# Kernel optimization log

Measured on AMD Instinct MI355X. Metric: run time of the kernel, lower is better.

The kernel has to match this reference:

```python
import jax, jax.numpy as jnp
import numpy as np

B, S, D, F, T, NS, L, H = 8, 1024, 1024, 4096, 64, 512, 32, 16
TAG_RATE = 0.5      # config.tagging_rate
GSR = 0.5           # config.gate_scaling_rate
ATT_EPS = 1e-12     # config.layer_norm_eps (att_norm)
ENC_EPS = 1e-5      # torch TransformerEncoderLayer default


def _ln(x, g, b, eps):
    m = x.mean(-1, keepdims=True)
    v = x.var(-1, keepdims=True)
    return (x - m) * jax.lax.rsqrt(v + eps) * g + b


def _rope(x):
    # standard rotary embedding over the full hidden dim
    d = x.shape[-1]
    s = x.shape[1]
    inv = 1.0 / (10000.0 ** (jnp.arange(0, d, 2, dtype=jnp.float32) / d))
    ang = jnp.arange(s, dtype=jnp.float32)[:, None] * inv[None, :]  # [S, D/2]
    sin, cos = jnp.sin(ang), jnp.cos(ang)
    x1, x2 = x[..., 0::2], x[..., 1::2]
    return jnp.stack([x1 * cos - x2 * sin, x1 * sin + x2 * cos], axis=-1).reshape(x.shape)


def setup_inputs() -> dict:
    key = jax.random.key(0)
    ks = jax.random.split(key, 24)
    p = lambda k, shp: (0.02 * jax.random.normal(k, shp, dtype=jnp.float32))
    inp = {
        'word_embedding': jax.random.normal(ks[0], (B, S, D), dtype=jnp.float32),
        'attention_mask': jnp.ones((B, S), dtype=jnp.int32),
        'span_batch': jax.random.randint(ks[1], (NS,), 0, B, dtype=jnp.int32),
        'span_start': jax.random.randint(ks[2], (NS,), 0, S - L, dtype=jnp.int32),
        'span_tag': jax.random.randint(ks[3], (NS,), 0, T, dtype=jnp.int32),
        'tag_emb': p(ks[4], (T, D)),
        'gate_w': p(ks[5], (D, 1)),
        'gate_b': jnp.zeros((1,), jnp.float32),
        'attn_ln_g': jnp.ones((D,), jnp.float32),
        'attn_ln_b': jnp.zeros((D,), jnp.float32),
        'in_proj_w': p(ks[6], (3 * D, D)),
        'in_proj_b': jnp.zeros((3 * D,), jnp.float32),
        'out_proj_w': p(ks[7], (D, D)),
        'out_proj_b': jnp.zeros((D,), jnp.float32),
        'enc_ln1_g': jnp.ones((D,), jnp.float32),
        'enc_ln1_b': jnp.zeros((D,), jnp.float32),
        'lin1_w': p(ks[8], (F, D)),
        'lin1_b': jnp.zeros((F,), jnp.float32),
        'lin2_w': p(ks[9], (D, F)),
        'lin2_b': jnp.zeros((D,), jnp.float32),
        'enc_ln2_g': jnp.ones((D,), jnp.float32),
        'enc_ln2_b': jnp.zeros((D,), jnp.float32),
    }
    return inp


def _mha(x, pad, in_proj_w, in_proj_b, out_proj_w, out_proj_b):
    b, s, d = x.shape
    hd = d // H
    qkv = x @ in_proj_w.T + in_proj_b                       # [B,S,3D]
    q, k, v = jnp.split(qkv, 3, axis=-1)
    rs = lambda t: t.reshape(b, s, H, hd).transpose(0, 2, 1, 3)  # [B,H,S,hd]
    q, k, v = rs(q), rs(k), rs(v)
    scores = jnp.einsum('bhqd,bhkd->bhqk', q, k) / jnp.sqrt(jnp.float32(hd))
    scores = jnp.where(pad[:, None, None, :], jnp.float32(-1e30), scores)
    attn = jax.nn.softmax(scores, axis=-1)
    o = jnp.einsum('bhqk,bhkd->bhqd', attn, v).transpose(0, 2, 1, 3).reshape(b, s, d)
    return o @ out_proj_w.T + out_proj_b


def reference(word_embedding, attention_mask, span_batch, span_start, span_tag,
              tag_emb, gate_w, gate_b, attn_ln_g, attn_ln_b,
              in_proj_w, in_proj_b, out_proj_w, out_proj_b,
              enc_ln1_g, enc_ln1_b, lin1_w, lin1_b, lin2_w, lin2_b,
              enc_ln2_g, enc_ln2_b):
    raw = word_embedding                        # dropout off (eval)
    we = _rope(word_embedding)
    # ragged gather -> gate -> scatter-add over fixed-length spans
    tok = span_start[:, None] + jnp.arange(L, dtype=jnp.int32)[None, :]  # [NS,L]
    X = we[span_batch[:, None], tok]            # [NS,L,D]
    gate = GSR * jax.nn.sigmoid(X @ gate_w + gate_b) + (1.0 - GSR) / 2.0  # [NS,L,1]
    res = gate * tag_emb[span_tag][:, None, :] * jnp.float32(L)          # [NS,L,D]
    taged = jnp.zeros_like(word_embedding).at[span_batch[:, None], tok].add(res)
    out_emb = raw + taged * TAG_RATE            # if_merge_by_add
    out_emb = _ln(out_emb, attn_ln_g, attn_ln_b, ATT_EPS)
    pad = attention_mask == 0
    # torch TransformerEncoderLayer (post-norm, relu)
    a = _mha(out_emb, pad, in_proj_w, in_proj_b, out_proj_w, out_proj_b)
    x = _ln(out_emb + a, enc_ln1_g, enc_ln1_b, ENC_EPS)
    ff = jax.nn.relu(x @ lin1_w.T + lin1_b) @ lin2_w.T + lin2_b
    enc = _ln(x + ff, enc_ln2_g, enc_ln2_b, ENC_EPS)
    return enc + out_emb
```

## Files before the change

### kernel.cpp

```cpp
#include <hip/hip_runtime.h>

#define DEV __device__ __forceinline__

typedef short bf16x8 __attribute__((ext_vector_type(8)));
typedef float f32x4 __attribute__((ext_vector_type(4)));
typedef unsigned short u16;
typedef unsigned int u32;

typedef __attribute__((address_space(3))) void lds_void;
typedef __attribute__((address_space(1))) void gbl_void;

DEV void async_copy16(void* lds_dst, const void* g_src) {
    __builtin_amdgcn_global_load_lds((gbl_void*)g_src, (lds_void*)lds_dst, 16, 0, 0);
}

DEV u16 f2bf(float x) {
    u32 u = __float_as_uint(x);
    return (u16)((u + 0x7fffu + ((u >> 16) & 1u)) >> 16);
}
DEV u16 f2bf_fast(float x) {
    return (u16)((__float_as_uint(x) + 0x8000u) >> 16);
}
DEV float bf2f(u16 v) { return __uint_as_float(((u32)v) << 16); }

__global__ __launch_bounds__(256) void f2bf_kernel(const float* __restrict__ src,
                                                   u16* __restrict__ dst, int n4) {
    const int i = blockIdx.x * 256 + threadIdx.x;
    if (i < n4) {
        const float4 v = ((const float4*)src)[i];
        ushort4 o;
        o.x = f2bf(v.x); o.y = f2bf(v.y); o.z = f2bf(v.z); o.w = f2bf(v.w);
        ((ushort4*)dst)[i] = o;
    }
}

__global__ __launch_bounds__(256) void span_kernel(
    const float* __restrict__ we, const int* __restrict__ sb,
    const int* __restrict__ ss, const int* __restrict__ stg,
    const float* __restrict__ tag_emb, const float* __restrict__ gate_w,
    const float* __restrict__ gate_b, float* __restrict__ out_pre) {
    __shared__ float red[4];
    const int n = blockIdx.x >> 5;
    const int l = blockIdx.x & 31;
    const int t = threadIdx.x;
    const int b = sb[n];
    const int s = ss[n] + l;
    const int tag = stg[n];
    const long base = ((long)b * 1024 + s) * 1024;
    float dot = 0.f;
#pragma unroll
    for (int pp = 0; pp < 2; ++pp) {
        const int p = t + pp * 256;
        const float e1 = we[base + 2 * p];
        const float e2 = we[base + 2 * p + 1];
        const float inv = exp2f((float)p * (-13.287712379549449f / 512.0f));
        const float ang = (float)s * inv;
        const float sa = sinf(ang), ca = cosf(ang);
        const float r1 = e1 * ca - e2 * sa;
        const float r2 = e1 * sa + e2 * ca;
        dot += r1 * gate_w[2 * p] + r2 * gate_w[2 * p + 1];
    }
#pragma unroll
    for (int off = 32; off > 0; off >>= 1) dot += __shfl_xor(dot, off, 64);
    if ((t & 63) == 0) red[t >> 6] = dot;
    __syncthreads();
    const float z = red[0] + red[1] + red[2] + red[3] + gate_b[0];
    const float gate = 0.25f + 0.5f / (1.f + __expf(-z));
    const float coef = gate * 16.f;
    const float* te = tag_emb + (long)tag * 1024;
#pragma unroll
    for (int c = 0; c < 4; ++c) {
        const int d = t + c * 256;
        atomicAdd(&out_pre[base + d], coef * te[d]);
    }
}

template <bool WRITE_F32, bool WRITE_BF, bool FINAL>
__global__ __launch_bounds__(256) void ln_kernel(
    const float* __restrict__ X, const float* __restrict__ g,
    const float* __restrict__ bta, float eps, float* __restrict__ Yf,
    u16* __restrict__ Ybf, const u16* __restrict__ addend) {
    __shared__ float red[8];
    const long row = blockIdx.x;
    const int t = threadIdx.x;
    const float4 x = ((const float4*)(X + row * 1024))[t];
    float s = x.x + x.y + x.z + x.w;
#pragma unroll
    for (int off = 32; off > 0; off >>= 1) s += __shfl_xor(s, off, 64);
    if ((t & 63) == 0) red[t >> 6] = s;
    __syncthreads();
    const float mean = (red[0] + red[1] + red[2] + red[3]) * (1.f / 1024.f);
    float4 dx;
    dx.x = x.x - mean; dx.y = x.y - mean; dx.z = x.z - mean; dx.w = x.w - mean;
    float ss = dx.x * dx.x + dx.y * dx.y + dx.z * dx.z + dx.w * dx.w;
#pragma unroll
    for (int off = 32; off > 0; off >>= 1) ss += __shfl_xor(ss, off, 64);
    if ((t & 63) == 0) red[4 + (t >> 6)] = ss;
    __syncthreads();
    const float var = (red[4] + red[5] + red[6] + red[7]) * (1.f / 1024.f);
    const float rstd = rsqrtf(var + eps);
    const float4 gv = ((const float4*)g)[t];
    const float4 bv = ((const float4*)bta)[t];
    float4 y;
    y.x = dx.x * rstd * gv.x + bv.x;
    y.y = dx.y * rstd * gv.y + bv.y;
    y.z = dx.z * rstd * gv.z + bv.z;
    y.w = dx.w * rstd * gv.w + bv.w;
    if (FINAL) {
        const ushort4 a = ((const ushort4*)(addend + row * 1024))[t];
        y.x += bf2f(a.x); y.y += bf2f(a.y); y.z += bf2f(a.z); y.w += bf2f(a.w);
    }
    if (WRITE_F32) ((float4*)(Yf + row * 1024))[t] = y;
    if (WRITE_BF) {
        ushort4 o;
        o.x = f2bf(y.x); o.y = f2bf(y.y); o.z = f2bf(y.z); o.w = f2bf(y.w);
        ((ushort4*)(Ybf + row * 1024))[t] = o;
    }
}

template <bool OUT_BF16, bool RELU, bool HAS_RES>
__global__ __launch_bounds__(256, 2) void gemm_nt(
    const u16* __restrict__ A, const u16* __restrict__ B,
    const float* __restrict__ bias, const u16* __restrict__ res,
    void* __restrict__ Cout, int N, int K) {
    __shared__ u16 Al[8192];
    __shared__ u16 Bl[8192];
    const int tid = threadIdx.x;
    const int wave = tid >> 6;
    const int lane = tid & 63;
    const int quad = lane >> 4;
    const int lq = lane & 15;
    const int wm = wave >> 1;
    const int wn = wave & 1;
    const long rowBase = (long)blockIdx.x * 128;
    const long colBase = (long)blockIdx.y * 128;

    f32x4 acc[4][4];
    const f32x4 fzero = {0.f, 0.f, 0.f, 0.f};
#pragma unroll
    for (int i = 0; i < 4; ++i)
#pragma unroll
        for (int j = 0; j < 4; ++j) acc[i][j] = fzero;

    const int rX = tid >> 3;
    const int pX = (tid & 7) ^ (rX & 7);
    const u16* gA = A + (rowBase + rX) * (long)K + pX * 8;
    const u16* gB = B + (colBase + rX) * (long)K + pX * 8;
    u16* ldsA = Al + wave * 512;
    u16* ldsB = Bl + wave * 512;

    for (int kt = 0; kt < K; kt += 64) {
        __syncthreads();
#pragma unroll
        for (int c = 0; c < 4; ++c) {
            async_copy16(ldsA + c * 2048, gA + (long)c * 32 * K + kt);
            async_copy16(ldsB + c * 2048, gB + (long)c * 32 * K + kt);
        }
        __syncthreads();
#pragma unroll
        for (int ks = 0; ks < 2; ++ks) {
            bf16x8 af[4], bfr[4];
#pragma unroll
            for (int i = 0; i < 4; ++i) {
                const int r = wm * 64 + i * 16 + lq;
                af[i] = *(const bf16x8*)&Al[r * 64 + (((ks * 4 + quad) ^ (lq & 7)) * 8)];
            }
#pragma unroll
            for (int j = 0; j < 4; ++j) {
                const int r = wn * 64 + j * 16 + lq;
                bfr[j] = *(const bf16x8*)&Bl[r * 64 + (((ks * 4 + quad) ^ (lq & 7)) * 8)];
            }
#pragma unroll
            for (int i = 0; i < 4; ++i)
#pragma unroll
                for (int j = 0; j < 4; ++j)
                    acc[i][j] = __builtin_amdgcn_mfma_f32_16x16x32_bf16(
                        af[i], bfr[j], acc[i][j], 0, 0, 0);
        }
    }

    float biasv[4];
#pragma unroll
    for (int j = 0; j < 4; ++j) biasv[j] = bias[colBase + wn * 64 + j * 16 + lq];
#pragma unroll
    for (int i = 0; i < 4; ++i) {
        const long grow = rowBase + wm * 64 + i * 16 + quad * 4;
#pragma unroll
        for (int j = 0; j < 4; ++j) {
            const long gcol = colBase + wn * 64 + j * 16 + lq;
#pragma unroll
            for (int r = 0; r < 4; ++r) {
                float v = acc[i][j][r] + biasv[j];
                if (RELU) v = fmaxf(v, 0.f);
                if (HAS_RES) v += bf2f(res[(grow + r) * N + gcol]);
                if (OUT_BF16)
                    ((u16*)Cout)[(grow + r) * N + gcol] = f2bf(v);
                else
                    ((float*)Cout)[(grow + r) * N + gcol] = v;
            }
        }
    }
}

#define PH_SYNC()                                          \
    do {                                                   \
        __builtin_amdgcn_s_barrier();                      \
        asm volatile("s_waitcnt lgkmcnt(0)" ::: "memory"); \
        __builtin_amdgcn_sched_barrier(0);                 \
    } while (0)

template <bool RELU>
__global__ __launch_bounds__(512, 2) void gemm_nt8(
    const u16* __restrict__ A, const u16* __restrict__ B,
    const float* __restrict__ bias, u16* __restrict__ Cout, int N, int K) {
    __shared__ u16 Al[2][16384];
    __shared__ u16 Bl[2][16384];
    const int tid = threadIdx.x;
    const int wave = tid >> 6;
    const int lane = tid & 63;
    const int quad = lane >> 4;
    const int lq = lane & 15;
    const int lq7 = lq & 7;
    const int wm = wave >> 2;
    const int wn = wave & 3;
    const long rowBase = (long)blockIdx.x * 256;
    const long colBase = (long)blockIdx.y * 256;
    const int NT = K >> 6;

    const int rs = tid >> 3;
    const int js = (tid & 7) ^ (rs & 7);
    const u16* gA = A + (rowBase + rs) * (long)K + js * 8;
    const u16* gB = B + (colBase + rs) * (long)K + js * 8;

    f32x4 acc[8][4];
    const f32x4 fz = {0.f, 0.f, 0.f, 0.f};
#pragma unroll
    for (int i = 0; i < 8; ++i)
#pragma unroll
        for (int j = 0; j < 4; ++j) acc[i][j] = fz;

    auto stA = [&](int buf, int h, int t) {
        u16* d = &Al[buf][h * 8192 + wave * 512];
        const u16* s = gA + (long)h * 128 * K + t * 64;
        async_copy16(d, s);
        async_copy16(d + 4096, s + (long)64 * K);
    };
    auto stB = [&](int buf, int h, int t) {
        u16* d = &Bl[buf][h * 8192 + wave * 512];
        const u16* s = gB + (long)h * 128 * K + t * 64;
        async_copy16(d, s);
        async_copy16(d + 4096, s + (long)64 * K);
    };
    auto ldA = [&](int buf, int i, int kh) {
        const int r = wm * 128 + i * 16 + lq;
        return *(const bf16x8*)&Al[buf][r * 64 + ((((kh << 2) | quad) ^ lq7) << 3)];
    };
    auto ldB = [&](int buf, int j, int kh) {
        const int r = wn * 64 + j * 16 + lq;
        return *(const bf16x8*)&Bl[buf][r * 64 + ((((kh << 2) | quad) ^ lq7) << 3)];
    };

    stA(0, 0, 0); stA(0, 1, 0); stB(0, 0, 0); stB(0, 1, 0);
    stA(1, 0, 1);
    asm volatile("s_waitcnt vmcnt(2)" ::: "memory");
    __builtin_amdgcn_s_barrier();

    bf16x8 at[8], ab[8], bl[4], br[4];
    for (int it = 0; it < (NT >> 1); ++it) {
        const int t1 = 2 * it + 1;
        int t2 = 2 * it + 2; if (t2 >= NT) t2 -= NT;
        int t3 = 2 * it + 3; if (t3 >= NT) t3 -= NT;

#pragma unroll
        for (int i = 0; i < 4; ++i) { at[2 * i] = ldA(0, i, 0); at[2 * i + 1] = ldA(0, i, 1); }
#pragma unroll
        for (int j = 0; j < 2; ++j) { bl[2 * j] = ldB(0, j, 0); bl[2 * j + 1] = ldB(0, j, 1); }
        stA(1, 1, t1);
        PH_SYNC();
        __builtin_amdgcn_s_setprio(1);
#pragma unroll
        for (int i = 0; i < 4; ++i)
#pragma unroll
            for (int j = 0; j < 2; ++j)
#pragma unroll
                for (int kh = 0; kh < 2; ++kh)
                    acc[i][j] = __builtin_amdgcn_mfma_f32_16x16x32_bf16(
                        at[2 * i + kh], bl[2 * j + kh], acc[i][j], 0, 0, 0);
        __builtin_amdgcn_s_setprio(0);
        __builtin_amdgcn_s_barrier();
#pragma unroll
        for (int j = 0; j < 2; ++j) { br[2 * j] = ldB(0, j + 2, 0); br[2 * j + 1] = ldB(0, j + 2, 1); }
        stB(1, 0, t1);
        PH_SYNC();
        __builtin_amdgcn_s_setprio(1);
#pragma unroll
        for (int i = 0; i < 4; ++i)
#pragma unroll
            for (int j = 0; j < 2; ++j)
#pragma unroll
                for (int kh = 0; kh < 2; ++kh)
                    acc[i][j + 2] = __builtin_amdgcn_mfma_f32_16x16x32_bf16(
                        at[2 * i + kh], br[2 * j + kh], acc[i][j + 2], 0, 0, 0);
        __builtin_amdgcn_s_setprio(0);
        __builtin_amdgcn_s_barrier();
#pragma unroll
        for (int i = 0; i < 4; ++i) { ab[2 * i] = ldA(0, i + 4, 0); ab[2 * i + 1] = ldA(0, i + 4, 1); }
        stB(1, 1, t1);
        PH_SYNC();
        __builtin_amdgcn_s_setprio(1);
#pragma unroll
        for (int i = 0; i < 4; ++i)
#pragma unroll
            for (int j = 0; j < 2; ++j)
#pragma unroll
                for (int kh = 0; kh < 2; ++kh)
                    acc[i + 4][j] = __builtin_amdgcn_mfma_f32_16x16x32_bf16(
                        ab[2 * i + kh], bl[2 * j + kh], acc[i + 4][j], 0, 0, 0);
        __builtin_amdgcn_s_setprio(0);
        __builtin_amdgcn_s_barrier();
        stA(0, 0, t2);
        PH_SYNC();
        __builtin_amdgcn_s_setprio(1);
#pragma unroll
        for (int i = 0; i < 4; ++i)
#pragma unroll
            for (int j = 0; j < 2; ++j)
#pragma unroll
                for (int kh = 0; kh < 2; ++kh)
                    acc[i + 4][j + 2] = __builtin_amdgcn_mfma_f32_16x16x32_bf16(
                        ab[2 * i + kh], br[2 * j + kh], acc[i + 4][j + 2], 0, 0, 0);
        __builtin_amdgcn_s_setprio(0);
        asm volatile("s_waitcnt vmcnt(2)" ::: "memory");
        __builtin_amdgcn_s_barrier();

#pragma unroll
        for (int i = 0; i < 4; ++i) { at[2 * i] = ldA(1, i, 0); at[2 * i + 1] = ldA(1, i, 1); }
#pragma unroll
        for (int j = 0; j < 2; ++j) { bl[2 * j] = ldB(1, j, 0); bl[2 * j + 1] = ldB(1, j, 1); }
        stA(0, 1, t2);
        PH_SYNC();
        __builtin_amdgcn_s_setprio(1);
#pragma unroll
        for (int i = 0; i < 4; ++i)
#pragma unroll
            for (int j = 0; j < 2; ++j)
#pragma unroll
                for (int kh = 0; kh < 2; ++kh)
                    acc[i][j] = __builtin_amdgcn_mfma_f32_16x16x32_bf16(
                        at[2 * i + kh], bl[2 * j + kh], acc[i][j], 0, 0, 0);
        __builtin_amdgcn_s_setprio(0);
        __builtin_amdgcn_s_barrier();
#pragma unroll
        for (int j = 0; j < 2; ++j) { br[2 * j] = ldB(1, j + 2, 0); br[2 * j + 1] = ldB(1, j + 2, 1); }
        stB(0, 0, t2);
        PH_SYNC();
        __builtin_amdgcn_s_setprio(1);
#pragma unroll
        for (int i = 0; i < 4; ++i)
#pragma unroll
            for (int j = 0; j < 2; ++j)
#pragma unroll
                for (int kh = 0; kh < 2; ++kh)
                    acc[i][j + 2] = __builtin_amdgcn_mfma_f32_16x16x32_bf16(
                        at[2 * i + kh], br[2 * j + kh], acc[i][j + 2], 0, 0, 0);
        __builtin_amdgcn_s_setprio(0);
        __builtin_amdgcn_s_barrier();
#pragma unroll
        for (int i = 0; i < 4; ++i) { ab[2 * i] = ldA(1, i + 4, 0); ab[2 * i + 1] = ldA(1, i + 4, 1); }
        stB(0, 1, t2);
        PH_SYNC();
        __builtin_amdgcn_s_setprio(1);
#pragma unroll
        for (int i = 0; i < 4; ++i)
#pragma unroll
            for (int j = 0; j < 2; ++j)
#pragma unroll
                for (int kh = 0; kh < 2; ++kh)
                    acc[i + 4][j] = __builtin_amdgcn_mfma_f32_16x16x32_bf16(
                        ab[2 * i + kh], bl[2 * j + kh], acc[i + 4][j], 0, 0, 0);
        __builtin_amdgcn_s_setprio(0);
        __builtin_amdgcn_s_barrier();
        stA(1, 0, t3);
        PH_SYNC();
        __builtin_amdgcn_s_setprio(1);
#pragma unroll
        for (int i = 0; i < 4; ++i)
#pragma unroll
            for (int j = 0; j < 2; ++j)
#pragma unroll
                for (int kh = 0; kh < 2; ++kh)
                    acc[i + 4][j + 2] = __builtin_amdgcn_mfma_f32_16x16x32_bf16(
                        ab[2 * i + kh], br[2 * j + kh], acc[i + 4][j + 2], 0, 0, 0);
        __builtin_amdgcn_s_setprio(0);
        asm volatile("s_waitcnt vmcnt(2)" ::: "memory");
        __builtin_amdgcn_s_barrier();
    }

    asm volatile("s_waitcnt vmcnt(0)" ::: "memory");
    float bv[4];
#pragma unroll
    for (int j = 0; j < 4; ++j) bv[j] = bias[colBase + wn * 64 + j * 16 + lq];
#pragma unroll
    for (int i = 0; i < 8; ++i) {
        const long grow = rowBase + wm * 128 + i * 16 + quad * 4;
#pragma unroll
        for (int j = 0; j < 4; ++j) {
            const long gcol = colBase + wn * 64 + j * 16 + lq;
#pragma unroll
            for (int r = 0; r < 4; ++r) {
                float v = acc[i][j][r] + bv[j];
                if (RELU) v = fmaxf(v, 0.f);
                Cout[(grow + r) * N + gcol] = f2bf(v);
            }
        }
    }
}

__global__ __launch_bounds__(256) void vtrans_kernel(const u16* __restrict__ QKV,
                                                     u16* __restrict__ Vt) {
    __shared__ u16 tile[64][72];
    const int bid = blockIdx.x;
    const int st = bid & 15;
    const int h = (bid >> 4) & 15;
    const int b = bid >> 8;
    const int t = threadIdx.x;
    const int sl = t >> 2;
    const int dc = (t & 3) * 16;
    const u16* src = QKV + ((long)(b * 1024 + st * 64 + sl)) * 3072 + 2048 + h * 64 + dc;
    *(uint4*)&tile[sl][dc] = *(const uint4*)src;
    *(uint4*)&tile[sl][dc + 8] = *(const uint4*)(src + 8);
    __syncthreads();
    const int dl = t >> 2;
    const int sc = (t & 3) * 16;
    union { u16 u[16]; uint4 q[2]; } tmp;
#pragma unroll
    for (int i = 0; i < 16; ++i) tmp.u[i] = tile[sc + i][dl];
    u16* dst = Vt + ((long)(b * 16 + h) * 64 + dl) * 1024 + st * 64 + sc;
    *(uint4*)dst = tmp.q[0];
    *(uint4*)(dst + 8) = tmp.q[1];
}

__global__ __launch_bounds__(256, 4) void attn_kernel(
    const u16* __restrict__ QKV, const u16* __restrict__ Vt,
    const int* __restrict__ mask, u16* __restrict__ Out) {
    __shared__ u16 KL[4096];
    __shared__ u16 VL[4096];
    __shared__ u16 PL[4][16 * 72];
    const int tid = threadIdx.x;
    const int wid = tid >> 6;
    const int lane = tid & 63;
    const int quad = lane >> 4;
    const int lq = lane & 15;
    const int slot0 = quad ^ (lq & 7);
    const int slot1 = slot0 ^ 4;

    const int bid = blockIdx.x;
    const int qb = bid & 7;
    const int h = (bid >> 3) & 15;
    const int b = bid >> 7;
    const int qbase = qb * 128 + wid * 32;

    bf16x8 aq[2][2];
#pragma unroll
    for (int t = 0; t < 2; ++t) {
        const u16* qp = QKV + ((long)(b * 1024 + qbase + t * 16 + lq)) * 3072 +
                        h * 64 + quad * 8;
        aq[t][0] = *(const bf16x8*)qp;
        aq[t][1] = *(const bf16x8*)(qp + 32);
    }

    const int c0 = tid, c1 = 256 + tid;
    const int r0 = c0 >> 3, j0 = (c0 & 7) ^ (r0 & 7);
    const int r1 = c1 >> 3, j1 = (c1 & 7) ^ (r1 & 7);
    const u16* srcK0 = QKV + ((long)(b * 1024 + r0)) * 3072 + 1024 + h * 64 + j0 * 8;
    const u16* srcK1 = QKV + ((long)(b * 1024 + r1)) * 3072 + 1024 + h * 64 + j1 * 8;
    const u16* srcV0 = Vt + ((long)(b * 16 + h) * 64 + r0) * 1024 + j0 * 8;
    const u16* srcV1 = Vt + ((long)(b * 16 + h) * 64 + r1) * 1024 + j1 * 8;
    u16* ldsK0 = KL + wid * 512;
    u16* ldsK1 = KL + 2048 + wid * 512;
    u16* ldsV0 = VL + wid * 512;
    u16* ldsV1 = VL + 2048 + wid * 512;

    const f32x4 fzero = {0.f, 0.f, 0.f, 0.f};
    f32x4 acc[2][4];
#pragma unroll
    for (int t = 0; t < 2; ++t)
#pragma unroll
        for (int j = 0; j < 4; ++j) acc[t][j] = fzero;
    float lsum[2][4] = {{0.f, 0.f, 0.f, 0.f}, {0.f, 0.f, 0.f, 0.f}};
    u16* myP = PL[wid];
    const int* mrow = mask + b * 1024;

    for (int kt = 0; kt < 1024; kt += 64) {
        __syncthreads();
        async_copy16(ldsK0, srcK0 + (long)kt * 3072);
        async_copy16(ldsK1, srcK1 + (long)kt * 3072);
        async_copy16(ldsV0, srcV0 + kt);
        async_copy16(ldsV1, srcV1 + kt);
        __syncthreads();

        bf16x8 kf0[4], kf1[4];
#pragma unroll
        for (int ct = 0; ct < 4; ++ct) {
            const int rowb = (ct * 16 + lq) * 64;
            kf0[ct] = *(const bf16x8*)&KL[rowb + slot0 * 8];
            kf1[ct] = *(const bf16x8*)&KL[rowb + slot1 * 8];
        }
        float mw[4];
#pragma unroll
        for (int ct = 0; ct < 4; ++ct) mw[ct] = mrow[kt + ct * 16 + lq] ? 1.f : 0.f;

#pragma unroll
        for (int t = 0; t < 2; ++t) {
            f32x4 s[4];
#pragma unroll
            for (int ct = 0; ct < 4; ++ct) {
                s[ct] = __builtin_amdgcn_mfma_f32_16x16x32_bf16(aq[t][0], kf0[ct],
                                                                fzero, 0, 0, 0);
                s[ct] = __builtin_amdgcn_mfma_f32_16x16x32_bf16(aq[t][1], kf1[ct],
                                                                s[ct], 0, 0, 0);
            }
            asm volatile("s_waitcnt lgkmcnt(0)" ::: "memory");
#pragma unroll
            for (int ct = 0; ct < 4; ++ct)
#pragma unroll
                for (int r = 0; r < 4; ++r) {
                    const float p = mw[ct] * __expf(s[ct][r] * 0.125f);
                    lsum[t][r] += p;
                    myP[(quad * 4 + r) * 72 + ct * 16 + lq] = f2bf_fast(p);
                }
            asm volatile("s_waitcnt lgkmcnt(0)" ::: "memory");
            const bf16x8 pf0 = *(const bf16x8*)&myP[lq * 72 + quad * 8];
            const bf16x8 pf1 = *(const bf16x8*)&myP[lq * 72 + 32 + quad * 8];
#pragma unroll
            for (int j = 0; j < 4; ++j) {
                const int rowb = (j * 16 + lq) * 64;
                const bf16x8 vf0 = *(const bf16x8*)&VL[rowb + slot0 * 8];
                const bf16x8 vf1 = *(const bf16x8*)&VL[rowb + slot1 * 8];
                acc[t][j] = __builtin_amdgcn_mfma_f32_16x16x32_bf16(pf0, vf0,
                                                                    acc[t][j], 0, 0, 0);
                acc[t][j] = __builtin_amdgcn_mfma_f32_16x16x32_bf16(pf1, vf1,
                                                                    acc[t][j], 0, 0, 0);
            }
        }
    }

#pragma unroll
    for (int t = 0; t < 2; ++t) {
        float inv[4];
#pragma unroll
        for (int r = 0; r < 4; ++r) {
            float l = lsum[t][r];
#pragma unroll
            for (int off = 1; off < 16; off <<= 1) l += __shfl_xor(l, off, 16);
            inv[r] = 1.f / l;
        }
        const long orow = (long)b * 1024 + qbase + t * 16 + quad * 4;
#pragma unroll
        for (int j = 0; j < 4; ++j)
#pragma unroll
            for (int r = 0; r < 4; ++r)
                Out[(orow + r) * 1024 + h * 64 + j * 16 + lq] =
                    f2bf_fast(acc[t][j][r] * inv[r]);
    }
}

extern "C" void kernel_launch(void* const* d_in, const int* in_sizes, int n_in,
                              void* d_out, int out_size, void* d_ws, size_t ws_size,
                              hipStream_t stream) {
    const float* we        = (const float*)d_in[0];
    const int*   amask     = (const int*)d_in[1];
    const int*   span_b    = (const int*)d_in[2];
    const int*   span_s    = (const int*)d_in[3];
    const int*   span_t    = (const int*)d_in[4];
    const float* tag_emb   = (const float*)d_in[5];
    const float* gate_w    = (const float*)d_in[6];
    const float* gate_b    = (const float*)d_in[7];
    const float* attn_ln_g = (const float*)d_in[8];
    const float* attn_ln_b = (const float*)d_in[9];
    const float* in_proj_w = (const float*)d_in[10];
    const float* in_proj_b = (const float*)d_in[11];
    const float* out_proj_w= (const float*)d_in[12];
    const float* out_proj_b= (const float*)d_in[13];
    const float* enc1_g    = (const float*)d_in[14];
    const float* enc1_b    = (const float*)d_in[15];
    const float* lin1_w    = (const float*)d_in[16];
    const float* lin1_b    = (const float*)d_in[17];
    const float* lin2_w    = (const float*)d_in[18];
    const float* lin2_b    = (const float*)d_in[19];
    const float* enc2_g    = (const float*)d_in[20];
    const float* enc2_b    = (const float*)d_in[21];
    float* out = (float*)d_out;

    char* ws = (char*)d_ws;
    size_t off = 0;
    auto alloc = [&](size_t bytes) {
        void* p = ws + off;
        off += (bytes + 255) & ~(size_t)255;
        return p;
    };
    const size_t MT = 8192;
    u16* oe_bf   = (u16*)alloc(MT * 1024 * 2);
    u16* ax_bf   = (u16*)alloc(MT * 1024 * 2);
    char* region = (char*)alloc((size_t)67108864);
    u16* qkv_bf  = (u16*)region;
    u16* vt_bf   = (u16*)(region + (size_t)MT * 3072 * 2);
    u16* ff1_bf  = (u16*)region;
    u16* wb_inproj  = (u16*)alloc((size_t)3072 * 1024 * 2);
    u16* wb_outproj = (u16*)alloc((size_t)1024 * 1024 * 2);
    u16* wb_lin1    = (u16*)alloc((size_t)4096 * 1024 * 2);
    u16* wb_lin2    = (u16*)alloc((size_t)1024 * 4096 * 2);

    hipMemcpyAsync(out, we, MT * 1024 * 4, hipMemcpyDeviceToDevice, stream);
    f2bf_kernel<<<3072, 256, 0, stream>>>(in_proj_w, wb_inproj, 3072 * 1024 / 4);
    f2bf_kernel<<<1024, 256, 0, stream>>>(out_proj_w, wb_outproj, 1024 * 1024 / 4);
    f2bf_kernel<<<4096, 256, 0, stream>>>(lin1_w, wb_lin1, 4096 * 1024 / 4);
    f2bf_kernel<<<4096, 256, 0, stream>>>(lin2_w, wb_lin2, 1024 * 4096 / 4);
    span_kernel<<<16384, 256, 0, stream>>>(we, span_b, span_s, span_t, tag_emb,
                                           gate_w, gate_b, out);
    ln_kernel<false, true, false><<<8192, 256, 0, stream>>>(
        out, attn_ln_g, attn_ln_b, 1e-12f, nullptr, oe_bf, nullptr);
    dim3 g1(32, 12);
    gemm_nt8<false><<<g1, 512, 0, stream>>>(oe_bf, wb_inproj, in_proj_b,
                                            qkv_bf, 3072, 1024);
    vtrans_kernel<<<2048, 256, 0, stream>>>(qkv_bf, vt_bf);
    attn_kernel<<<1024, 256, 0, stream>>>(qkv_bf, vt_bf, amask, ax_bf);
    dim3 g2(64, 8);
    gemm_nt<false, false, true><<<g2, 256, 0, stream>>>(ax_bf, wb_outproj, out_proj_b,
                                                        oe_bf, out, 1024, 1024);
    ln_kernel<false, true, false><<<8192, 256, 0, stream>>>(
        out, enc1_g, enc1_b, 1e-5f, nullptr, ax_bf, nullptr);
    dim3 g3(32, 16);
    gemm_nt8<true><<<g3, 512, 0, stream>>>(ax_bf, wb_lin1, lin1_b,
                                           ff1_bf, 4096, 1024);
    gemm_nt<false, false, true><<<g2, 256, 0, stream>>>(ff1_bf, wb_lin2, lin2_b,
                                                        ax_bf, out, 1024, 4096);
    ln_kernel<true, false, true><<<8192, 256, 0, stream>>>(
        out, enc2_g, enc2_b, 1e-5f, out, nullptr, oe_bf);
}
```

Measured before the change: 570.1 us.

## Replace simple NT GEMM with triple-buffered 256x128 pipelined kernel; reorder gemm_nt8 prefetch

The out-projection and lin2 GEMMs move from a single-buffered 128x128 kernel, which waits on two barriers every K step, to a new 512-thread 256x128 kernel. The new kernel keeps three LDS stages and prefetches two tiles ahead so global loads overlap MFMA work. The existing gemm_nt8 also gets a reordered prefetch schedule: B halves are loaded earlier, the wait counts are relaxed, and the sched_barrier is dropped from the sync macro. The grid for these GEMMs halves to 256 blocks, which may underfill the GPU.

```diff
diff --git a/kernel.cpp b/kernel.cpp
--- a/kernel.cpp
+++ b/kernel.cpp
@@ -118,96 +118,12 @@
     }
 }
 
-template <bool OUT_BF16, bool RELU, bool HAS_RES>
-__global__ __launch_bounds__(256, 2) void gemm_nt(
-    const u16* __restrict__ A, const u16* __restrict__ B,
-    const float* __restrict__ bias, const u16* __restrict__ res,
-    void* __restrict__ Cout, int N, int K) {
-    __shared__ u16 Al[8192];
-    __shared__ u16 Bl[8192];
-    const int tid = threadIdx.x;
-    const int wave = tid >> 6;
-    const int lane = tid & 63;
-    const int quad = lane >> 4;
-    const int lq = lane & 15;
-    const int wm = wave >> 1;
-    const int wn = wave & 1;
-    const long rowBase = (long)blockIdx.x * 128;
-    const long colBase = (long)blockIdx.y * 128;
-
-    f32x4 acc[4][4];
-    const f32x4 fzero = {0.f, 0.f, 0.f, 0.f};
-#pragma unroll
-    for (int i = 0; i < 4; ++i)
-#pragma unroll
-        for (int j = 0; j < 4; ++j) acc[i][j] = fzero;
-
-    const int rX = tid >> 3;
-    const int pX = (tid & 7) ^ (rX & 7);
-    const u16* gA = A + (rowBase + rX) * (long)K + pX * 8;
-    const u16* gB = B + (colBase + rX) * (long)K + pX * 8;
-    u16* ldsA = Al + wave * 512;
-    u16* ldsB = Bl + wave * 512;
-
-    for (int kt = 0; kt < K; kt += 64) {
-        __syncthreads();
-#pragma unroll
-        for (int c = 0; c < 4; ++c) {
-            async_copy16(ldsA + c * 2048, gA + (long)c * 32 * K + kt);
-            async_copy16(ldsB + c * 2048, gB + (long)c * 32 * K + kt);
-        }
-        __syncthreads();
-#pragma unroll
-        for (int ks = 0; ks < 2; ++ks) {
-            bf16x8 af[4], bfr[4];
-#pragma unroll
-            for (int i = 0; i < 4; ++i) {
-                const int r = wm * 64 + i * 16 + lq;
-                af[i] = *(const bf16x8*)&Al[r * 64 + (((ks * 4 + quad) ^ (lq & 7)) * 8)];
-            }
-#pragma unroll
-            for (int j = 0; j < 4; ++j) {
-                const int r = wn * 64 + j * 16 + lq;
-                bfr[j] = *(const bf16x8*)&Bl[r * 64 + (((ks * 4 + quad) ^ (lq & 7)) * 8)];
-            }
-#pragma unroll
-            for (int i = 0; i < 4; ++i)
-#pragma unroll
-                for (int j = 0; j < 4; ++j)
-                    acc[i][j] = __builtin_amdgcn_mfma_f32_16x16x32_bf16(
-                        af[i], bfr[j], acc[i][j], 0, 0, 0);
-        }
-    }
-
-    float biasv[4];
-#pragma unroll
-    for (int j = 0; j < 4; ++j) biasv[j] = bias[colBase + wn * 64 + j * 16 + lq];
-#pragma unroll
-    for (int i = 0; i < 4; ++i) {
-        const long grow = rowBase + wm * 64 + i * 16 + quad * 4;
-#pragma unroll
-        for (int j = 0; j < 4; ++j) {
-            const long gcol = colBase + wn * 64 + j * 16 + lq;
-#pragma unroll
-            for (int r = 0; r < 4; ++r) {
-                float v = acc[i][j][r] + biasv[j];
-                if (RELU) v = fmaxf(v, 0.f);
-                if (HAS_RES) v += bf2f(res[(grow + r) * N + gcol]);
-                if (OUT_BF16)
-                    ((u16*)Cout)[(grow + r) * N + gcol] = f2bf(v);
-                else
-                    ((float*)Cout)[(grow + r) * N + gcol] = v;
-            }
-        }
-    }
-}
-
 #define PH_SYNC()                                          \
     do {                                                   \
         __builtin_amdgcn_s_barrier();                      \
         asm volatile("s_waitcnt lgkmcnt(0)" ::: "memory"); \
-        __builtin_amdgcn_sched_barrier(0);                 \
     } while (0)
+#define PH_CLOSE() asm volatile("s_barrier" ::: "memory")
 
 template <bool RELU>
 __global__ __launch_bounds__(512, 2) void gemm_nt8(
@@ -241,13 +157,13 @@
 
     auto stA = [&](int buf, int h, int t) {
         u16* d = &Al[buf][h * 8192 + wave * 512];
-        const u16* s = gA + (long)h * 128 * K + t * 64;
+        const u16* s = gA + (long)h * 128 * K + (long)t * 64;
         async_copy16(d, s);
         async_copy16(d + 4096, s + (long)64 * K);
     };
     auto stB = [&](int buf, int h, int t) {
         u16* d = &Bl[buf][h * 8192 + wave * 512];
-        const u16* s = gB + (long)h * 128 * K + t * 64;
+        const u16* s = gB + (long)h * 128 * K + (long)t * 64;
         async_copy16(d, s);
         async_copy16(d + 4096, s + (long)64 * K);
     };
@@ -261,9 +177,9 @@
     };
 
     stA(0, 0, 0); stA(0, 1, 0); stB(0, 0, 0); stB(0, 1, 0);
-    stA(1, 0, 1);
-    asm volatile("s_waitcnt vmcnt(2)" ::: "memory");
-    __builtin_amdgcn_s_barrier();
+    stB(1, 0, 1); stB(1, 1, 1);
+    asm volatile("s_waitcnt vmcnt(4)" ::: "memory");
+    PH_CLOSE();
 
     bf16x8 at[8], ab[8], bl[4], br[4];
     for (int it = 0; it < (NT >> 1); ++it) {
@@ -275,7 +191,7 @@
         for (int i = 0; i < 4; ++i) { at[2 * i] = ldA(0, i, 0); at[2 * i + 1] = ldA(0, i, 1); }
 #pragma unroll
         for (int j = 0; j < 2; ++j) { bl[2 * j] = ldB(0, j, 0); bl[2 * j + 1] = ldB(0, j, 1); }
-        stA(1, 1, t1);
+        stA(1, 0, t1);
         PH_SYNC();
         __builtin_amdgcn_s_setprio(1);
 #pragma unroll
@@ -287,10 +203,10 @@
                     acc[i][j] = __builtin_amdgcn_mfma_f32_16x16x32_bf16(
                         at[2 * i + kh], bl[2 * j + kh], acc[i][j], 0, 0, 0);
         __builtin_amdgcn_s_setprio(0);
-        __builtin_amdgcn_s_barrier();
+        PH_CLOSE();
 #pragma unroll
         for (int j = 0; j < 2; ++j) { br[2 * j] = ldB(0, j + 2, 0); br[2 * j + 1] = ldB(0, j + 2, 1); }
-        stB(1, 0, t1);
+        stA(1, 1, t1);
         PH_SYNC();
         __builtin_amdgcn_s_setprio(1);
 #pragma unroll
@@ -302,10 +218,10 @@
                     acc[i][j + 2] = __builtin_amdgcn_mfma_f32_16x16x32_bf16(
                         at[2 * i + kh], br[2 * j + kh], acc[i][j + 2], 0, 0, 0);
         __builtin_amdgcn_s_setprio(0);
-        __builtin_amdgcn_s_barrier();
+        PH_CLOSE();
 #pragma unroll
         for (int i = 0; i < 4; ++i) { ab[2 * i] = ldA(0, i + 4, 0); ab[2 * i + 1] = ldA(0, i + 4, 1); }
-        stB(1, 1, t1);
+        stB(0, 0, t2);
         PH_SYNC();
         __builtin_amdgcn_s_setprio(1);
 #pragma unroll
@@ -317,8 +233,8 @@
                     acc[i + 4][j] = __builtin_amdgcn_mfma_f32_16x16x32_bf16(
                         ab[2 * i + kh], bl[2 * j + kh], acc[i + 4][j], 0, 0, 0);
         __builtin_amdgcn_s_setprio(0);
-        __builtin_amdgcn_s_barrier();
-        stA(0, 0, t2);
+        PH_CLOSE();
+        stB(0, 1, t2);
         PH_SYNC();
         __builtin_amdgcn_s_setprio(1);
 #pragma unroll
@@ -330,14 +246,14 @@
                     acc[i + 4][j + 2] = __builtin_amdgcn_mfma_f32_16x16x32_bf16(
                         ab[2 * i + kh], br[2 * j + kh], acc[i + 4][j + 2], 0, 0, 0);
         __builtin_amdgcn_s_setprio(0);
-        asm volatile("s_waitcnt vmcnt(2)" ::: "memory");
-        __builtin_amdgcn_s_barrier();
+        asm volatile("s_waitcnt vmcnt(4)" ::: "memory");
+        PH_CLOSE();
 
 #pragma unroll
         for (int i = 0; i < 4; ++i) { at[2 * i] = ldA(1, i, 0); at[2 * i + 1] = ldA(1, i, 1); }
 #pragma unroll
         for (int j = 0; j < 2; ++j) { bl[2 * j] = ldB(1, j, 0); bl[2 * j + 1] = ldB(1, j, 1); }
-        stA(0, 1, t2);
+        stA(0, 0, t2);
         PH_SYNC();
         __builtin_amdgcn_s_setprio(1);
 #pragma unroll
@@ -349,10 +265,10 @@
                     acc[i][j] = __builtin_amdgcn_mfma_f32_16x16x32_bf16(
                         at[2 * i + kh], bl[2 * j + kh], acc[i][j], 0, 0, 0);
         __builtin_amdgcn_s_setprio(0);
-        __builtin_amdgcn_s_barrier();
+        PH_CLOSE();
 #pragma unroll
         for (int j = 0; j < 2; ++j) { br[2 * j] = ldB(1, j + 2, 0); br[2 * j + 1] = ldB(1, j + 2, 1); }
-        stB(0, 0, t2);
+        stA(0, 1, t2);
         PH_SYNC();
         __builtin_amdgcn_s_setprio(1);
 #pragma unroll
@@ -364,10 +280,10 @@
                     acc[i][j + 2] = __builtin_amdgcn_mfma_f32_16x16x32_bf16(
                         at[2 * i + kh], br[2 * j + kh], acc[i][j + 2], 0, 0, 0);
         __builtin_amdgcn_s_setprio(0);
-        __builtin_amdgcn_s_barrier();
+        PH_CLOSE();
 #pragma unroll
         for (int i = 0; i < 4; ++i) { ab[2 * i] = ldA(1, i + 4, 0); ab[2 * i + 1] = ldA(1, i + 4, 1); }
-        stB(0, 1, t2);
+        stB(1, 0, t3);
         PH_SYNC();
         __builtin_amdgcn_s_setprio(1);
 #pragma unroll
@@ -379,8 +295,8 @@
                     acc[i + 4][j] = __builtin_amdgcn_mfma_f32_16x16x32_bf16(
                         ab[2 * i + kh], bl[2 * j + kh], acc[i + 4][j], 0, 0, 0);
         __builtin_amdgcn_s_setprio(0);
-        __builtin_amdgcn_s_barrier();
-        stA(1, 0, t3);
+        PH_CLOSE();
+        stB(1, 1, t3);
         PH_SYNC();
         __builtin_amdgcn_s_setprio(1);
 #pragma unroll
@@ -392,8 +308,8 @@
                     acc[i + 4][j + 2] = __builtin_amdgcn_mfma_f32_16x16x32_bf16(
                         ab[2 * i + kh], br[2 * j + kh], acc[i + 4][j + 2], 0, 0, 0);
         __builtin_amdgcn_s_setprio(0);
-        asm volatile("s_waitcnt vmcnt(2)" ::: "memory");
-        __builtin_amdgcn_s_barrier();
+        asm volatile("s_waitcnt vmcnt(4)" ::: "memory");
+        PH_CLOSE();
     }
 
     asm volatile("s_waitcnt vmcnt(0)" ::: "memory");
@@ -411,6 +327,127 @@
                 float v = acc[i][j][r] + bv[j];
                 if (RELU) v = fmaxf(v, 0.f);
                 Cout[(grow + r) * N + gcol] = f2bf(v);
+            }
+        }
+    }
+}
+
+template <bool OUT_BF16, bool RELU, bool HAS_RES>
+__global__ __launch_bounds__(512, 2) void gemm_nt8b(
+    const u16* __restrict__ A, const u16* __restrict__ B,
+    const float* __restrict__ bias, const u16* __restrict__ res,
+    void* __restrict__ Cout, int N, int K) {
+    __shared__ u16 LT[3][24576];
+    const int tid = threadIdx.x;
+    const int wave = tid >> 6;
+    const int lane = tid & 63;
+    const int quad = lane >> 4;
+    const int lq = lane & 15;
+    const int lq7 = lq & 7;
+    const int wm = wave >> 1;
+    const int wn = wave & 1;
+    const long rowBase = (long)blockIdx.x * 256;
+    const long colBase = (long)blockIdx.y * 128;
+    const int NT = K >> 6;
+
+    const int rs = tid >> 3;
+    const int js = (tid & 7) ^ (rs & 7);
+    const u16* gA = A + (rowBase + rs) * (long)K + js * 8;
+    const u16* gB = B + (colBase + rs) * (long)K + js * 8;
+    const long s64K = (long)64 * K;
+
+    f32x4 acc[4][4];
+    const f32x4 fz = {0.f, 0.f, 0.f, 0.f};
+#pragma unroll
+    for (int i = 0; i < 4; ++i)
+#pragma unroll
+        for (int j = 0; j < 4; ++j) acc[i][j] = fz;
+
+    auto stage = [&](int so, int u, int t) {
+        u16* d = &LT[0][0] + so + u * 4096 + wave * 512;
+        const u16* s = (u < 4 ? gA + u * s64K : gB + (u - 4) * s64K) + (long)t * 64;
+        async_copy16(d, s);
+    };
+    auto ldA = [&](int bo, int i, int kh) {
+        const int r = wm * 64 + i * 16 + lq;
+        return *(const bf16x8*)(&LT[0][0] + bo + r * 64 +
+                                ((((kh << 2) | quad) ^ lq7) << 3));
+    };
+    auto ldB = [&](int bo, int j, int kh) {
+        const int r = wn * 64 + j * 16 + lq;
+        return *(const bf16x8*)(&LT[0][0] + bo + 16384 + r * 64 +
+                                ((((kh << 2) | quad) ^ lq7) << 3));
+    };
+
+#pragma unroll
+    for (int u = 0; u < 6; ++u) stage(0, u, 0);
+#pragma unroll
+    for (int u = 0; u < 6; ++u) stage(24576, u, 1);
+    asm volatile("s_waitcnt vmcnt(6)" ::: "memory");
+    __builtin_amdgcn_s_barrier();
+
+    int bo = 0;
+    int so = 2 * 24576;
+    for (int t = 0; t < NT; ++t) {
+        int tp2 = t + 2;
+        if (tp2 >= NT) tp2 -= NT;
+        bf16x8 a8[8], bb[8];
+#pragma unroll
+        for (int i = 0; i < 4; ++i) { a8[2 * i] = ldA(bo, i, 0); a8[2 * i + 1] = ldA(bo, i, 1); }
+#pragma unroll
+        for (int j = 0; j < 2; ++j) { bb[2 * j] = ldB(bo, j, 0); bb[2 * j + 1] = ldB(bo, j, 1); }
+        stage(so, 0, tp2); stage(so, 1, tp2); stage(so, 2, tp2);
+        PH_SYNC();
+        __builtin_amdgcn_s_setprio(1);
+#pragma unroll
+        for (int i = 0; i < 4; ++i)
+#pragma unroll
+            for (int j = 0; j < 2; ++j)
+#pragma unroll
+                for (int kh = 0; kh < 2; ++kh)
+                    acc[i][j] = __builtin_amdgcn_mfma_f32_16x16x32_bf16(
+                        a8[2 * i + kh], bb[2 * j + kh], acc[i][j], 0, 0, 0);
+        __builtin_amdgcn_s_setprio(0);
+        PH_CLOSE();
+#pragma unroll
+        for (int j = 0; j < 2; ++j) { bb[4 + 2 * j] = ldB(bo, j + 2, 0); bb[4 + 2 * j + 1] = ldB(bo, j + 2, 1); }
+        stage(so, 3, tp2); stage(so, 4, tp2); stage(so, 5, tp2);
+        PH_SYNC();
+        __builtin_amdgcn_s_setprio(1);
+#pragma unroll
+        for (int i = 0; i < 4; ++i)
+#pragma unroll
+            for (int j = 0; j < 2; ++j)
+#pragma unroll
+                for (int kh = 0; kh < 2; ++kh)
+                    acc[i][j + 2] = __builtin_amdgcn_mfma_f32_16x16x32_bf16(
+                        a8[2 * i + kh], bb[4 + 2 * j + kh], acc[i][j + 2], 0, 0, 0);
+        __builtin_amdgcn_s_setprio(0);
+        asm volatile("s_waitcnt vmcnt(6)" ::: "memory");
+        PH_CLOSE();
+        bo += 24576; if (bo == 3 * 24576) bo = 0;
+        so += 24576; if (so == 3 * 24576) so = 0;
+    }
+
+    asm volatile("s_waitcnt vmcnt(0)" ::: "memory");
+    float bv[4];
+#pragma unroll
+    for (int j = 0; j < 4; ++j) bv[j] = bias[colBase + wn * 64 + j * 16 + lq];
+#pragma unroll
+    for (int i = 0; i < 4; ++i) {
+        const long grow = rowBase + wm * 64 + i * 16 + quad * 4;
+#pragma unroll
+        for (int j = 0; j < 4; ++j) {
+            const long gcol = colBase + wn * 64 + j * 16 + lq;
+#pragma unroll
+            for (int r = 0; r < 4; ++r) {
+                float v = acc[i][j][r] + bv[j];
+                if (RELU) v = fmaxf(v, 0.f);
+                if (HAS_RES) v += bf2f(res[(grow + r) * N + gcol]);
+                if (OUT_BF16)
+                    ((u16*)Cout)[(grow + r) * N + gcol] = f2bf(v);
+                else
+                    ((float*)Cout)[(grow + r) * N + gcol] = v;
             }
         }
     }
@@ -625,16 +662,16 @@
                                             qkv_bf, 3072, 1024);
     vtrans_kernel<<<2048, 256, 0, stream>>>(qkv_bf, vt_bf);
     attn_kernel<<<1024, 256, 0, stream>>>(qkv_bf, vt_bf, amask, ax_bf);
-    dim3 g2(64, 8);
-    gemm_nt<false, false, true><<<g2, 256, 0, stream>>>(ax_bf, wb_outproj, out_proj_b,
-                                                        oe_bf, out, 1024, 1024);
+    dim3 g2(32, 8);
+    gemm_nt8b<false, false, true><<<g2, 512, 0, stream>>>(
+        ax_bf, wb_outproj, out_proj_b, oe_bf, out, 1024, 1024);
     ln_kernel<false, true, false><<<8192, 256, 0, stream>>>(
         out, enc1_g, enc1_b, 1e-5f, nullptr, ax_bf, nullptr);
     dim3 g3(32, 16);
     gemm_nt8<true><<<g3, 512, 0, stream>>>(ax_bf, wb_lin1, lin1_b,
                                            ff1_bf, 4096, 1024);
-    gemm_nt<false, false, true><<<g2, 256, 0, stream>>>(ff1_bf, wb_lin2, lin2_b,
-                                                        ax_bf, out, 1024, 4096);
+    gemm_nt8b<false, false, true><<<g2, 512, 0, stream>>>(
+        ff1_bf, wb_lin2, lin2_b, ax_bf, out, 1024, 4096);
     ln_kernel<true, false, true><<<8192, 256, 0, stream>>>(
         out, enc2_g, enc2_b, 1e-5f, out, nullptr, oe_bf);
 }
```

After: 568.8 us. Within noise of the previous version (-0.2%).
